# Performance work log

Hardware: AMD Instinct MI355X
Metric: run time of the kernel (lower is better)

The kernel has to match this reference:

```python
import jax, jax.numpy as jnp
from jax import lax
import numpy as np

BLOCKS = 6
DIM = 768
D_STATE = 16
D_CONV = 4
EXPAND = 2
HEADDIM = 64
D_INNER = EXPAND * DIM              # 1536
NHEADS = D_INNER // HEADDIM        # 24
CONV_DIM = D_INNER + 2 * D_STATE   # 1568 (ngroups=1)
D_IN_PROJ = 2 * D_INNER + 2 * D_STATE + NHEADS  # 3128
NPITCH = 128


def setup_inputs() -> dict:
    key = jax.random.key(0)
    ks = jax.random.split(key, 16)
    B, L = 4, 4096
    s = 0.02
    return {
        "x": jax.random.normal(ks[0], (B, L, DIM), jnp.float32),
        "type_IDs": jax.random.randint(ks[1], (B, L), 0, 2),
        "in_proj_w": jax.random.normal(ks[2], (BLOCKS, D_IN_PROJ, DIM), jnp.float32) * s,
        "conv_w": jax.random.normal(ks[3], (BLOCKS, CONV_DIM, D_CONV), jnp.float32) * 0.1,
        "conv_b": jnp.zeros((BLOCKS, CONV_DIM), jnp.float32),
        "dt_bias": jax.random.uniform(ks[4], (BLOCKS, NHEADS), jnp.float32, -4.0, -2.0),
        "A_log": jnp.tile(jnp.log(jnp.linspace(1.0, 16.0, NHEADS, dtype=jnp.float32)), (BLOCKS, 1)),
        "D": jnp.ones((BLOCKS, NHEADS), jnp.float32),
        "norm_w": jnp.ones((BLOCKS, D_INNER), jnp.float32),
        "out_proj_w": jax.random.normal(ks[5], (BLOCKS, DIM, D_INNER), jnp.float32) * s,
        "head_w": jax.random.normal(ks[6], (2, DIM, DIM), jnp.float32) * s,
        "head_b": jnp.zeros((2, DIM), jnp.float32),
        "head_out_w": jax.random.normal(ks[7], (2, 4, NPITCH, DIM), jnp.float32) * s,
        "head_out_b": jnp.zeros((2, 4, NPITCH), jnp.float32),
    }


def _mamba2_block(x, Wi, cw, cb, dtb, Alog, Dp, nw, Wo):
    B, L, _ = x.shape
    zxbcdt = jnp.einsum('bld,ed->ble', x, Wi)                 # [B,L,D_IN_PROJ]
    z = zxbcdt[..., :D_INNER]
    xBC = zxbcdt[..., D_INNER:D_INNER + CONV_DIM]
    dt = zxbcdt[..., -NHEADS:]
    # causal depthwise conv1d over time
    xc = jnp.pad(jnp.swapaxes(xBC, 1, 2), ((0, 0), (0, 0), (D_CONV - 1, 0)))
    xBC = lax.conv_general_dilated(xc, cw[:, None, :], (1,), 'VALID',
                                   feature_group_count=CONV_DIM,
                                   dimension_numbers=('NCH', 'OIH', 'NCH'))
    xBC = jax.nn.silu(jnp.swapaxes(xBC, 1, 2) + cb)            # [B,L,CONV_DIM]
    xs = xBC[..., :D_INNER].reshape(B, L, NHEADS, HEADDIM)
    Bm = xBC[..., D_INNER:D_INNER + D_STATE]                   # [B,L,N]
    Cm = xBC[..., D_INNER + D_STATE:]                          # [B,L,N]
    dt = jax.nn.softplus(dt + dtb)                             # [B,L,H]
    dA = jnp.exp(dt * (-jnp.exp(Alog)))                        # [B,L,H]
    dtx = dt[..., None] * xs                                   # [B,L,H,P]

    def step(h, inp):
        dA_t, dtx_t, B_t, C_t = inp
        h = h * dA_t[:, :, None, None] + dtx_t[..., None] * B_t[:, None, None, :]
        y = jnp.einsum('bhpn,bn->bhp', h, C_t)
        return h, y

    h0 = jnp.zeros((B, NHEADS, HEADDIM, D_STATE), x.dtype)
    mv = lambda a: jnp.moveaxis(a, 1, 0)
    _, ys = lax.scan(step, h0, (mv(dA), mv(dtx), mv(Bm), mv(Cm)))
    y = jnp.moveaxis(ys, 0, 1) + Dp[None, None, :, None] * xs   # [B,L,H,P]
    y = y.reshape(B, L, D_INNER) * jax.nn.silu(z)               # gated
    y = y * lax.rsqrt(jnp.mean(y * y, -1, keepdims=True) + 1e-5) * nw
    return jnp.einsum('bli,di->bld', y, Wo)


def _head(t, hw, hb, ow, ob):
    h = jnp.einsum('bld,ed->ble', t, hw) + hb
    velocity = jnp.einsum('bld,pd->blp', h, ow[0]) + ob[0]
    onset = jax.nn.sigmoid(jnp.einsum('bld,pd->blp', h, ow[1]) + ob[1])
    offset = jax.nn.sigmoid(jnp.einsum('bld,pd->blp', h, ow[2]) + ob[2])
    frames = jax.nn.sigmoid(jnp.einsum('bld,pd->blp', h, ow[3]) + ob[3])
    return velocity, frames, onset, offset


def reference(x, type_IDs, in_proj_w, conv_w, conv_b, dt_bias, A_log, D,
              norm_w, out_proj_w, head_w, head_b, head_out_w, head_out_b):
    for i in range(BLOCKS):
        x = _mamba2_block(x, in_proj_w[i], conv_w[i], conv_b[i], dt_bias[i],
                          A_log[i], D[i], norm_w[i], out_proj_w[i])
    cmask = (type_IDs == 0).astype(x.dtype)[..., None]
    fmask = (type_IDs == 1).astype(x.dtype)[..., None]
    cv, cf, con, coff = _head(x, head_w[0], head_b[0], head_out_w[0], head_out_b[0])
    fv, ff, fon, foff = _head(x, head_w[1], head_b[1], head_out_w[1], head_out_b[1])
    # masked (instead of ragged boolean gather) to stay jit-compatible
    return jnp.stack([cv * cmask, cf * cmask, con * cmask, coff * cmask,
                      fv * fmask, ff * fmask, fon * fmask, foff * fmask])
```

## Files before the change

kernel.cpp:

```cpp
#include <hip/hip_runtime.h>
#include <cstdint>
#include <cstddef>

#define L_SEQ   4096
#define BATCH   4
#define DIMM    768
#define D_INNER 1536
#define NHEADS  24
#define HEADDIM 64
#define D_STATE 16
#define CONVD   1568
#define D_IPROJ 3128
#define ZXP     3200
#define SEGLEN  64
#define NSEG    (L_SEQ / SEGLEN)

typedef _Float16 f16x8 __attribute__((ext_vector_type(8)));
typedef _Float16 f16x4 __attribute__((ext_vector_type(4)));
typedef float    f32x4 __attribute__((ext_vector_type(4)));

__device__ __forceinline__ void glds16(const _Float16* g, _Float16* l) {
  __builtin_amdgcn_global_load_lds(
      (__attribute__((address_space(1))) unsigned int*)g,
      (__attribute__((address_space(3))) unsigned int*)l, 16, 0, 0);
}

template <int OM>
__global__ __launch_bounds__(256, 2) void gemm_mfma(
    const _Float16* __restrict__ A, int lda,
    const _Float16* __restrict__ W,
    const float* __restrict__ bias,
    void* __restrict__ Cv, long ldc, long extra,
    int M, int N, int K,
    const int* __restrict__ tidsp, int thead)
{
  __shared__ __align__(16) char smem[33792];
  _Float16* As = (_Float16*)smem;
  _Float16* Ws = (_Float16*)(smem + 16384);
  const int tid = threadIdx.x;
  const int lane = tid & 63, wid = tid >> 6;
  const int wr = wid >> 1, wc = wid & 1;

  const int nbx = gridDim.x, nby = gridDim.y;
  const int flat = blockIdx.y * nbx + blockIdx.x;
  const int xcd = flat & 7;
  const int bidx = flat >> 3;
  const int rpx = nby >> 3;
  const int rl = bidx % rpx;
  const int ct = bidx / rpx;
  const long m0 = (long)(xcd * rpx + rl) * 128;
  const int n0 = ct * 128;

  const int la = lane & 15, lg = lane >> 4;
  const int srow = lane >> 3, schunk = lane & 7;

  f32x4 acc[4][4] = {};

  for (int k0 = 0; k0 < K; k0 += 64) {
    __syncthreads();
#pragma unroll
    for (int p = 0; p < 4; ++p) {
      const int rg = (wid << 2) + p;
      const int row = (rg << 3) + srow;
      const int scn = schunk ^ (row & 7);
      glds16(A + (m0 + row) * (long)lda + k0 + scn * 8, As + rg * 512);
      int n = n0 + row; if (n >= N) n = N - 1;
      glds16(W + (long)n * K + k0 + scn * 8, Ws + rg * 512);
    }
    asm volatile("s_waitcnt vmcnt(0)" ::: "memory");
    __syncthreads();
#pragma unroll
    for (int ks = 0; ks < 2; ++ks) {
      const int cc = ks * 4 + lg;
      f16x8 af[4], bfr[4];
#pragma unroll
      for (int i = 0; i < 4; ++i) {
        int ra = wr * 64 + i * 16 + la;
        int rb = wc * 64 + i * 16 + la;
        af[i]  = *(const f16x8*)&As[ra * 64 + ((cc ^ (ra & 7)) << 3)];
        bfr[i] = *(const f16x8*)&Ws[rb * 64 + ((cc ^ (rb & 7)) << 3)];
      }
#pragma unroll
      for (int i = 0; i < 4; ++i)
#pragma unroll
        for (int j = 0; j < 4; ++j)
          acc[i][j] = __builtin_amdgcn_mfma_f32_16x16x32_f16(af[i], bfr[j], acc[i][j], 0, 0, 0);
    }
  }

  float* epi = (float*)smem;
#pragma unroll
  for (int ph = 0; ph < 2; ++ph) {
    __syncthreads();
    if (wr == ph) {
#pragma unroll
      for (int i = 0; i < 4; ++i)
#pragma unroll
        for (int j = 0; j < 4; ++j)
#pragma unroll
          for (int r = 0; r < 4; ++r)
            epi[(i * 16 + lg * 4 + r) * 132 + wc * 64 + j * 16 + la] = acc[i][j][r];
    }
    __syncthreads();
    if (OM == 3) {
      const int q = n0 >> 7;
      const int rr = tid >> 5;
      const int ch = tid & 31;
#pragma unroll
      for (int ps = 0; ps < 8; ++ps) {
        int lrow = ps * 8 + rr;
        long gr = m0 + ph * 64 + lrow;
        float keep = (tidsp[gr] == thead) ? 1.f : 0.f;
        float4 v = *(float4*)&epi[lrow * 132 + ch * 4];
        float o[4] = {v.x, v.y, v.z, v.w};
#pragma unroll
        for (int e = 0; e < 4; ++e) {
          float vv = o[e] + bias[n0 + ch * 4 + e];
          if (q != 0) vv = 1.f / (1.f + expf(-vv));
          o[e] = vv * keep;
        }
        *(float4*)((float*)Cv + (long)q * extra + gr * 128 + ch * 4) =
            make_float4(o[0], o[1], o[2], o[3]);
      }
    } else {
      const int rr = tid >> 4;
      const int ch = tid & 15;
      const int col = n0 + ch * 8;
      float b[8] = {0.f, 0.f, 0.f, 0.f, 0.f, 0.f, 0.f, 0.f};
      if (OM == 2 && col < N) {
#pragma unroll
        for (int e = 0; e < 8; ++e) b[e] = bias[col + e];
      }
#pragma unroll
      for (int ps = 0; ps < 4; ++ps) {
        int lrow = ps * 16 + rr;
        long gr = m0 + ph * 64 + lrow;
        if (col < N) {
          float4 v0 = *(float4*)&epi[lrow * 132 + ch * 8];
          float4 v1 = *(float4*)&epi[lrow * 132 + ch * 8 + 4];
          f16x8 o = {(_Float16)(v0.x + b[0]), (_Float16)(v0.y + b[1]),
                     (_Float16)(v0.z + b[2]), (_Float16)(v0.w + b[3]),
                     (_Float16)(v1.x + b[4]), (_Float16)(v1.y + b[5]),
                     (_Float16)(v1.z + b[6]), (_Float16)(v1.w + b[7])};
          *(f16x8*)((_Float16*)Cv + gr * ldc + col) = o;
        }
      }
    }
  }
}

__global__ __launch_bounds__(256) void cvt_kernel(
    const float* __restrict__ src, _Float16* __restrict__ dst, long n4)
{
  long i = (long)blockIdx.x * 256 + threadIdx.x;
  long stride = (long)gridDim.x * 256;
  for (; i < n4; i += stride) {
    float4 v = *(const float4*)(src + i * 4);
    f16x4 o = { (_Float16)v.x, (_Float16)v.y, (_Float16)v.z, (_Float16)v.w };
    *(f16x4*)(dst + i * 4) = o;
  }
}

__global__ __launch_bounds__(256) void pack_head_kernel(
    const float* __restrict__ how, const float* __restrict__ hob,
    _Float16* __restrict__ howb, float* __restrict__ hobp)
{
  const int wmap[4] = {0, 3, 1, 2};
  int idx = blockIdx.x * 256 + threadIdx.x;
  if (idx < 2 * 512 * 768) {
    int t = idx / (512 * 768);
    int rem = idx - t * 512 * 768;
    int q = rem / (128 * 768);
    int rem2 = rem - q * 128 * 768;
    howb[idx] = (_Float16)how[((size_t)(t * 4 + wmap[q])) * 128 * 768 + rem2];
  }
  if (idx < 1024) {
    int t = idx >> 9, rem = idx & 511;
    int q = rem >> 7, pp = rem & 127;
    hobp[idx] = hob[(t * 4 + wmap[q]) * 128 + pp];
  }
}

__global__ __launch_bounds__(64) void ssdA_kernel(
    const _Float16* __restrict__ zx, const float* __restrict__ cw,
    const float* __restrict__ cb, const float* __restrict__ dtb,
    const float* __restrict__ alog, const float* __restrict__ Dv,
    _Float16* __restrict__ ybuf, _Float16* __restrict__ bcbuf,
    float* __restrict__ Hseg, float* __restrict__ cumq)
{
  __shared__ __align__(16) char sm[30720];
  _Float16* Mr = (_Float16*)sm;
  _Float16* XT = (_Float16*)(sm + 8192);
  _Float16* XC = (_Float16*)(sm + 16384);
  _Float16* BC = (_Float16*)(sm + 24832);
  float* sdt = (float*)(sm + 29952);
  float* sa  = (float*)(sm + 30208);
  float* sw  = (float*)(sm + 30464);
  const int lane = threadIdx.x;
  const int seg = blockIdx.x & (NSEG - 1);
  const int bh = blockIdx.x >> 6;
  const int h = bh % NHEADS, b = bh / NHEADS;
  const int bl0 = b * L_SEQ + seg * SEGLEN;

  _Float16* bcraw = Mr;
  for (int i = lane; i < 67 * 4; i += 64) {
    int r = i >> 2, q = (i & 3) << 3;
    f16x8 v = {};
    if (seg > 0 || r >= 3)
      v = *(const f16x8*)&zx[(size_t)(bl0 - 3 + r) * ZXP + 2 * D_INNER + q];
    *(f16x8*)&bcraw[r * 32 + q] = v;
  }
  {
    float raw = (float)zx[(size_t)(bl0 + lane) * ZXP + (D_INNER + CONVD) + h] + dtb[h];
    float sp = (raw > 20.f) ? raw : log1pf(expf(raw));
    sdt[lane] = sp;
    float av = expf(alog[h]) * sp;
#pragma unroll
    for (int off = 1; off < 64; off <<= 1) {
      float tv = __shfl_up(av, off, 64);
      if (lane >= off) av += tv;
    }
    sa[lane] = av;
    cumq[(size_t)bh * L_SEQ + seg * SEGLEN + lane] = expf(-av);
    float alast = __shfl(av, 63, 64);
    sw[lane] = expf(av - alast);
  }
  __syncthreads();

  for (int i = lane; i < SEGLEN * 32; i += 64) {
    int t = i >> 5, c = i & 31;
    float acc = cb[D_INNER + c];
#pragma unroll
    for (int k = 0; k < 4; ++k)
      acc = fmaf(cw[(D_INNER + c) * 4 + k], (float)bcraw[(t + k) * 32 + c], acc);
    float s = acc / (1.f + expf(-acc));
    _Float16 sh = (_Float16)s;
    BC[t * 40 + c] = sh;
    bcbuf[(size_t)(bl0 + t) * 32 + c] = sh;
  }
  __syncthreads();

  const int xch = h * HEADDIM + lane;
  const _Float16* xg = zx + (size_t)bl0 * ZXP + D_INNER + xch;
  const float cwx0 = cw[xch * 4 + 0], cwx1 = cw[xch * 4 + 1];
  const float cwx2 = cw[xch * 4 + 2], cwx3 = cw[xch * 4 + 3];
  const float cbx = cb[xch];
  float xw0 = 0.f, xw1 = 0.f, xw2 = 0.f;
  if (seg > 0) {
    xw0 = (float)xg[-3 * (long)ZXP];
    xw1 = (float)xg[-2 * (long)ZXP];
    xw2 = (float)xg[-1 * (long)ZXP];
  }
  float xcur = (float)xg[0];
  for (int t = 0; t < SEGLEN; ++t) {
    float xnext = (t < SEGLEN - 1) ? (float)xg[(size_t)(t + 1) * ZXP] : 0.f;
    float xa = cbx;
    xa = fmaf(cwx0, xw0, xa);
    xa = fmaf(cwx1, xw1, xa);
    xa = fmaf(cwx2, xw2, xa);
    xa = fmaf(cwx3, xcur, xa);
    float xv = xa / (1.f + expf(-xa));
    XC[t * 66 + lane] = (_Float16)xv;
    float dtx = sdt[t] * xv;
    XT[lane * 64 + ((((t >> 3) ^ (lane & 7))) << 3) + (t & 7)] = (_Float16)dtx;
    xw0 = xw1; xw1 = xw2; xw2 = xcur; xcur = xnext;
  }
  __syncthreads();

  const int la = lane & 15, lg = lane >> 4;

  f32x4 acc1[4][4] = {};
  {
    f16x8 af[4], bf[4];
#pragma unroll
    for (int i = 0; i < 4; ++i) {
      f16x8 v = {};
      if (lg < 2) v = *(const f16x8*)&BC[(i * 16 + la) * 40 + 16 + lg * 8];
      af[i] = v;
    }
#pragma unroll
    for (int j = 0; j < 4; ++j) {
      f16x8 v = {};
      if (lg < 2) v = *(const f16x8*)&BC[(j * 16 + la) * 40 + lg * 8];
      bf[j] = v;
    }
#pragma unroll
    for (int i = 0; i < 4; ++i)
#pragma unroll
      for (int j = 0; j < 4; ++j)
        acc1[i][j] = __builtin_amdgcn_mfma_f32_16x16x32_f16(af[i], bf[j], acc1[i][j], 0, 0, 0);
  }
#pragma unroll
  for (int i = 0; i < 4; ++i)
#pragma unroll
    for (int j = 0; j < 4; ++j)
#pragma unroll
      for (int r = 0; r < 4; ++r) {
        int t = i * 16 + lg * 4 + r, s = j * 16 + la;
        float m = 0.f;
        if (s <= t) m = acc1[i][j][r] * expf(sa[s] - sa[t]);
        Mr[t * 64 + ((((s >> 3) ^ (t & 7))) << 3) + (s & 7)] = (_Float16)m;
      }
  __syncthreads();

  f32x4 acc2[4][4] = {};
#pragma unroll
  for (int ks = 0; ks < 2; ++ks) {
    const int cc = ks * 4 + lg;
    f16x8 am[4], wx[4];
#pragma unroll
    for (int i = 0; i < 4; ++i) {
      int rt = i * 16 + la;
      am[i] = *(const f16x8*)&Mr[rt * 64 + ((cc ^ (rt & 7)) << 3)];
    }
#pragma unroll
    for (int j = 0; j < 4; ++j) {
      int rp = j * 16 + la;
      wx[j] = *(const f16x8*)&XT[rp * 64 + ((cc ^ (rp & 7)) << 3)];
    }
#pragma unroll
    for (int i = 0; i < 4; ++i)
#pragma unroll
      for (int j = 0; j < 4; ++j)
        acc2[i][j] = __builtin_amdgcn_mfma_f32_16x16x32_f16(am[i], wx[j], acc2[i][j], 0, 0, 0);
  }
  const float Dh = Dv[h];
#pragma unroll
  for (int i = 0; i < 4; ++i)
#pragma unroll
    for (int j = 0; j < 4; ++j)
#pragma unroll
      for (int r = 0; r < 4; ++r) {
        int t = i * 16 + lg * 4 + r, p = j * 16 + la;
        float y = acc2[i][j][r] + Dh * (float)XC[t * 66 + p];
        ybuf[(size_t)(bl0 + t) * D_INNER + h * HEADDIM + p] = (_Float16)y;
      }

  f32x4 acc3[4] = {};
#pragma unroll
  for (int ks = 0; ks < 2; ++ks) {
    const int cc = ks * 4 + lg;
    f16x8 b3;
#pragma unroll
    for (int e = 0; e < 8; ++e)
      b3[e] = BC[(ks * 32 + lg * 8 + e) * 40 + la];
#pragma unroll
    for (int i = 0; i < 4; ++i) {
      int rp = i * 16 + la;
      f16x8 a3 = *(const f16x8*)&XT[rp * 64 + ((cc ^ (rp & 7)) << 3)];
      f16x8 a3w;
#pragma unroll
      for (int e = 0; e < 8; ++e)
        a3w[e] = (_Float16)((float)a3[e] * sw[ks * 32 + lg * 8 + e]);
      acc3[i] = __builtin_amdgcn_mfma_f32_16x16x32_f16(a3w, b3, acc3[i], 0, 0, 0);
    }
  }
  float* Hst = Hseg + ((size_t)bh * NSEG + seg) * 1024;
#pragma unroll
  for (int i = 0; i < 4; ++i)
#pragma unroll
    for (int r = 0; r < 4; ++r) {
      int p = i * 16 + lg * 4 + r;
      Hst[p * 16 + la] = acc3[i][r];
    }
}

__global__ __launch_bounds__(1024) void scanB_kernel(
    float* __restrict__ Hseg, const float* __restrict__ cumq)
{
  const int bh = blockIdx.x;
  const int t = threadIdx.x;
  __shared__ float sp[NSEG];
  if (t < NSEG) sp[t] = cumq[(size_t)bh * L_SEQ + t * SEGLEN + (SEGLEN - 1)];
  __syncthreads();
  float v[NSEG];
#pragma unroll
  for (int s = 0; s < NSEG; ++s)
    v[s] = Hseg[((size_t)bh * NSEG + s) * 1024 + t];
  float h = 0.f;
#pragma unroll
  for (int s = 0; s < NSEG; ++s) {
    Hseg[((size_t)bh * NSEG + s) * 1024 + t] = h;
    h = fmaf(sp[s], h, v[s]);
  }
}

__global__ __launch_bounds__(64) void ssdC_kernel(
    _Float16* __restrict__ ybuf, const _Float16* __restrict__ bcbuf,
    const float* __restrict__ Hseg, const float* __restrict__ cumq)
{
  const int seg = blockIdx.x & (NSEG - 1);
  if (seg == 0) return;
  const int lane = threadIdx.x;
  const int bh = blockIdx.x >> 6;
  const int h = bh % NHEADS, b = bh / NHEADS;
  const int bl0 = b * L_SEQ + seg * SEGLEN;
  __shared__ float scq[SEGLEN];
  scq[lane] = cumq[(size_t)bh * L_SEQ + seg * SEGLEN + lane];
  const int la = lane & 15, lg = lane >> 4;
  const float* slot = Hseg + ((size_t)bh * NSEG + seg) * 1024;

  f16x8 a4[4], w4[4];
#pragma unroll
  for (int i = 0; i < 4; ++i) {
    f16x8 v = {};
    if (lg < 2)
      v = *(const f16x8*)&bcbuf[(size_t)(bl0 + i * 16 + la) * 32 + 16 + lg * 8];
    a4[i] = v;
  }
#pragma unroll
  for (int j = 0; j < 4; ++j) {
    f16x8 v = {};
    if (lg < 2) {
#pragma unroll
      for (int e = 0; e < 8; ++e)
        v[e] = (_Float16)slot[(j * 16 + la) * 16 + lg * 8 + e];
    }
    w4[j] = v;
  }
  f32x4 acc[4][4] = {};
#pragma unroll
  for (int i = 0; i < 4; ++i)
#pragma unroll
    for (int j = 0; j < 4; ++j)
      acc[i][j] = __builtin_amdgcn_mfma_f32_16x16x32_f16(a4[i], w4[j], acc[i][j], 0, 0, 0);
  __syncthreads();
#pragma unroll
  for (int i = 0; i < 4; ++i)
#pragma unroll
    for (int j = 0; j < 4; ++j)
#pragma unroll
      for (int r = 0; r < 4; ++r) {
        int t = i * 16 + lg * 4 + r, p = j * 16 + la;
        size_t ad = (size_t)(bl0 + t) * D_INNER + h * HEADDIM + p;
        ybuf[ad] = (_Float16)((float)ybuf[ad] + scq[t] * acc[i][j][r]);
      }
}

__global__ __launch_bounds__(256) void norm_kernel(
    const _Float16* __restrict__ y, _Float16* __restrict__ zx,
    const float* __restrict__ nw)
{
  const int row = blockIdx.x;
  const int tid = threadIdx.x;
  const _Float16* yr = y + (size_t)row * D_INNER;
  _Float16* zr = zx + (size_t)row * ZXP;
  float v[6];
  float ss = 0.f;
#pragma unroll
  for (int jj = 0; jj < 6; ++jj) {
    int c = jj * 256 + tid;
    float yv = (float)yr[c];
    float zv = (float)zr[c];
    float sz = zv / (1.f + expf(-zv));
    float val = yv * sz;
    v[jj] = val;
    ss = fmaf(val, val, ss);
  }
#pragma unroll
  for (int off = 32; off > 0; off >>= 1) ss += __shfl_xor(ss, off, 64);
  __shared__ float red[4];
  if ((tid & 63) == 0) red[tid >> 6] = ss;
  __syncthreads();
  float tot = red[0] + red[1] + red[2] + red[3];
  float rs = rsqrtf(tot * (1.f / 1536.f) + 1e-5f);
#pragma unroll
  for (int jj = 0; jj < 6; ++jj) {
    int c = jj * 256 + tid;
    zr[c] = (_Float16)(v[jj] * rs * nw[c]);
  }
}

extern "C" void kernel_launch(void* const* d_in, const int* in_sizes, int n_in,
                              void* d_out, int out_size, void* d_ws, size_t ws_size,
                              hipStream_t stream)
{
  const float* x_in = (const float*)d_in[0];
  const int*   tids = (const int*)d_in[1];
  const float* ipw  = (const float*)d_in[2];
  const float* cw   = (const float*)d_in[3];
  const float* cb   = (const float*)d_in[4];
  const float* dtb  = (const float*)d_in[5];
  const float* alog = (const float*)d_in[6];
  const float* Dv   = (const float*)d_in[7];
  const float* nw   = (const float*)d_in[8];
  const float* opw  = (const float*)d_in[9];
  const float* hw   = (const float*)d_in[10];
  const float* hb   = (const float*)d_in[11];
  const float* how  = (const float*)d_in[12];
  const float* hob  = (const float*)d_in[13];
  float* out = (float*)d_out;

  char* p = (char*)d_ws;
  _Float16* ipw_b = (_Float16*)p; p += (size_t)14413824 * 2;
  _Float16* opw_b = (_Float16*)p; p += (size_t)7077888 * 2;
  _Float16* hw_b  = (_Float16*)p; p += (size_t)1179648 * 2;
  _Float16* how_b = (_Float16*)p; p += (size_t)786432 * 2;
  float*    hob_p = (float*)p;    p += (size_t)1024 * 4;
  const size_t used_w = (size_t)(p - (char*)d_ws);
  const size_t PB = 54528000;
  int nb = 4;
  while (nb > 1 && used_w + (size_t)nb * PB > ws_size) nb >>= 1;

  cvt_kernel<<<8192, 256, 0, stream>>>(ipw, ipw_b, 14413824 / 4);
  cvt_kernel<<<6912, 256, 0, stream>>>(opw, opw_b, 7077888 / 4);
  cvt_kernel<<<1152, 256, 0, stream>>>(hw, hw_b, 1179648 / 4);
  pack_head_kernel<<<3072, 256, 0, stream>>>(how, hob, how_b, hob_p);

  for (int b0 = 0; b0 < BATCH; b0 += nb) {
    const int MT = nb * L_SEQ;
    _Float16* zx    = (_Float16*)p;
    _Float16* ybuf  = zx + (size_t)MT * ZXP;
    _Float16* bcbuf = ybuf + (size_t)MT * D_INNER;
    float*    Hseg  = (float*)(bcbuf + (size_t)MT * 32);
    float*    cumq  = Hseg + (size_t)nb * NHEADS * NSEG * 1024;
    _Float16* xbuf  = (_Float16*)(cumq + (size_t)MT * NHEADS);
    _Float16* hbuf  = zx;

    cvt_kernel<<<6144, 256, 0, stream>>>(x_in + (size_t)b0 * L_SEQ * DIMM,
                                         xbuf, (long)MT * DIMM / 4);

    for (int i = 0; i < 6; ++i) {
      gemm_mfma<0><<<dim3((D_IPROJ + 127) / 128, MT / 128), 256, 0, stream>>>(
          xbuf, DIMM, ipw_b + (size_t)i * D_IPROJ * DIMM, nullptr,
          zx, ZXP, 0, MT, D_IPROJ, DIMM, nullptr, 0);
      ssdA_kernel<<<nb * NHEADS * NSEG, 64, 0, stream>>>(
          zx, cw + (size_t)i * CONVD * 4, cb + i * CONVD,
          dtb + i * NHEADS, alog + i * NHEADS, Dv + i * NHEADS,
          ybuf, bcbuf, Hseg, cumq);
      scanB_kernel<<<nb * NHEADS, 1024, 0, stream>>>(Hseg, cumq);
      ssdC_kernel<<<nb * NHEADS * NSEG, 64, 0, stream>>>(ybuf, bcbuf, Hseg, cumq);
      norm_kernel<<<MT, 256, 0, stream>>>(ybuf, zx, nw + i * D_INNER);
      gemm_mfma<0><<<dim3(DIMM / 128, MT / 128), 256, 0, stream>>>(
          zx, ZXP, opw_b + (size_t)i * DIMM * D_INNER, nullptr,
          xbuf, DIMM, 0, MT, DIMM, D_INNER, nullptr, 0);
    }

    for (int t = 0; t < 2; ++t) {
      gemm_mfma<2><<<dim3(DIMM / 128, MT / 128), 256, 0, stream>>>(
          xbuf, DIMM, hw_b + (size_t)t * DIMM * DIMM, hb + t * DIMM,
          hbuf, DIMM, 0, MT, DIMM, DIMM, nullptr, 0);
      gemm_mfma<3><<<dim3(4, MT / 128), 256, 0, stream>>>(
          hbuf, DIMM, how_b + (size_t)t * 512 * DIMM, hob_p + t * 512,
          out + (size_t)t * 4 * 16384 * 128 + (size_t)b0 * L_SEQ * 128,
          128, (long)16384 * 128, MT, 512, DIMM,
          tids + (size_t)b0 * L_SEQ, t);
    }
  }
}
```

Baseline: 2.110 ms.

## Keep SSD intra-chunk mask in registers and shrink ssdA shared memory

The ssdA kernel now computes the masked C·B^T decay matrix with 16x16x16 MFMAs laid out so the result fragments feed the next MFMA straight from registers, removing the Mr shared-memory round trip and its barrier. The transposed dt-scaled x buffer and the separate copy of x are replaced by one XV buffer. The dt and decay scalings are applied on the fly when operands are built, with the decay weight pre-multiplied by dt. Shared memory per block drops from about 30KB to 14KB, which should allow more resident blocks. The cost is more register pressure from holding 16 fragments and more scalar conversion work when building operands.

```diff
diff --git a/kernel.cpp b/kernel.cpp
--- a/kernel.cpp
+++ b/kernel.cpp
@@ -188,21 +188,19 @@
     _Float16* __restrict__ ybuf, _Float16* __restrict__ bcbuf,
     float* __restrict__ Hseg, float* __restrict__ cumq)
 {
-  __shared__ __align__(16) char sm[30720];
-  _Float16* Mr = (_Float16*)sm;
-  _Float16* XT = (_Float16*)(sm + 8192);
-  _Float16* XC = (_Float16*)(sm + 16384);
-  _Float16* BC = (_Float16*)(sm + 24832);
-  float* sdt = (float*)(sm + 29952);
-  float* sa  = (float*)(sm + 30208);
-  float* sw  = (float*)(sm + 30464);
+  __shared__ __align__(16) char sm[14336];
+  _Float16* XV    = (_Float16*)sm;
+  _Float16* bcraw = (_Float16*)sm;
+  _Float16* BC    = (_Float16*)(sm + 8448);
+  float* sa  = (float*)(sm + 13568);
+  float* sdt = (float*)(sm + 13824);
+  float* sws = (float*)(sm + 14080);
   const int lane = threadIdx.x;
   const int seg = blockIdx.x & (NSEG - 1);
   const int bh = blockIdx.x >> 6;
   const int h = bh % NHEADS, b = bh / NHEADS;
   const int bl0 = b * L_SEQ + seg * SEGLEN;
 
-  _Float16* bcraw = Mr;
   for (int i = lane; i < 67 * 4; i += 64) {
     int r = i >> 2, q = (i & 3) << 3;
     f16x8 v = {};
@@ -223,7 +221,7 @@
     sa[lane] = av;
     cumq[(size_t)bh * L_SEQ + seg * SEGLEN + lane] = expf(-av);
     float alast = __shfl(av, 63, 64);
-    sw[lane] = expf(av - alast);
+    sws[lane] = expf(av - alast) * sp;
   }
   __syncthreads();
 
@@ -259,110 +257,93 @@
     xa = fmaf(cwx1, xw1, xa);
     xa = fmaf(cwx2, xw2, xa);
     xa = fmaf(cwx3, xcur, xa);
-    float xv = xa / (1.f + expf(-xa));
-    XC[t * 66 + lane] = (_Float16)xv;
-    float dtx = sdt[t] * xv;
-    XT[lane * 64 + ((((t >> 3) ^ (lane & 7))) << 3) + (t & 7)] = (_Float16)dtx;
+    XV[t * 66 + lane] = (_Float16)(xa / (1.f + expf(-xa)));
     xw0 = xw1; xw1 = xw2; xw2 = xcur; xcur = xnext;
   }
   __syncthreads();
 
   const int la = lane & 15, lg = lane >> 4;
 
-  f32x4 acc1[4][4] = {};
+  f16x4 Mfrag[4][4];
   {
-    f16x8 af[4], bf[4];
-#pragma unroll
-    for (int i = 0; i < 4; ++i) {
-      f16x8 v = {};
-      if (lg < 2) v = *(const f16x8*)&BC[(i * 16 + la) * 40 + 16 + lg * 8];
-      af[i] = v;
-    }
-#pragma unroll
-    for (int j = 0; j < 4; ++j) {
-      f16x8 v = {};
-      if (lg < 2) v = *(const f16x8*)&BC[(j * 16 + la) * 40 + lg * 8];
-      bf[j] = v;
-    }
-#pragma unroll
-    for (int i = 0; i < 4; ++i)
-#pragma unroll
-      for (int j = 0; j < 4; ++j)
-        acc1[i][j] = __builtin_amdgcn_mfma_f32_16x16x32_f16(af[i], bf[j], acc1[i][j], 0, 0, 0);
-  }
-#pragma unroll
-  for (int i = 0; i < 4; ++i)
-#pragma unroll
-    for (int j = 0; j < 4; ++j)
+    f16x4 cf[4];
+    float sat[4];
+#pragma unroll
+    for (int tt = 0; tt < 4; ++tt) {
+      cf[tt] = *(const f16x4*)&BC[(tt * 16 + la) * 40 + 16 + lg * 4];
+      sat[tt] = sa[tt * 16 + la];
+    }
+#pragma unroll
+    for (int st = 0; st < 4; ++st) {
+      f16x4 bfA = *(const f16x4*)&BC[(st * 16 + la) * 40 + lg * 4];
+#pragma unroll
+      for (int tt = 0; tt < 4; ++tt) {
+        f32x4 a1 = {};
+        a1 = __builtin_amdgcn_mfma_f32_16x16x16f16(bfA, cf[tt], a1, 0, 0, 0);
+        f16x4 m;
+#pragma unroll
+        for (int r = 0; r < 4; ++r) {
+          int s = st * 16 + lg * 4 + r;
+          int t = tt * 16 + la;
+          float mv = 0.f;
+          if (s <= t) mv = a1[r] * expf(sa[s] - sat[tt]);
+          m[r] = (_Float16)mv;
+        }
+        Mfrag[st][tt] = m;
+      }
+    }
+  }
+
+  f16x4 b3[4];
+#pragma unroll
+  for (int st = 0; st < 4; ++st) {
+    f16x4 v;
+#pragma unroll
+    for (int e = 0; e < 4; ++e)
+      v[e] = BC[(st * 16 + lg * 4 + e) * 40 + la];
+    b3[st] = v;
+  }
+
+  const float Dh = Dv[h];
+  float* Hst = Hseg + ((size_t)bh * NSEG + seg) * 1024;
+#pragma unroll
+  for (int pt = 0; pt < 4; ++pt) {
+    f16x4 bf[4], af3[4];
+#pragma unroll
+    for (int st = 0; st < 4; ++st) {
+      f16x4 v, w;
+#pragma unroll
+      for (int e = 0; e < 4; ++e) {
+        int s = st * 16 + lg * 4 + e;
+        float xv = (float)XV[s * 66 + pt * 16 + la];
+        v[e] = (_Float16)(xv * sdt[s]);
+        w[e] = (_Float16)(xv * sws[s]);
+      }
+      bf[st] = v; af3[st] = w;
+    }
+#pragma unroll
+    for (int tt = 0; tt < 4; ++tt) {
+      f32x4 a2 = {};
+#pragma unroll
+      for (int st = 0; st < 4; ++st)
+        a2 = __builtin_amdgcn_mfma_f32_16x16x16f16(Mfrag[st][tt], bf[st], a2, 0, 0, 0);
 #pragma unroll
       for (int r = 0; r < 4; ++r) {
-        int t = i * 16 + lg * 4 + r, s = j * 16 + la;
-        float m = 0.f;
-        if (s <= t) m = acc1[i][j][r] * expf(sa[s] - sa[t]);
-        Mr[t * 64 + ((((s >> 3) ^ (t & 7))) << 3) + (s & 7)] = (_Float16)m;
-      }
-  __syncthreads();
-
-  f32x4 acc2[4][4] = {};
-#pragma unroll
-  for (int ks = 0; ks < 2; ++ks) {
-    const int cc = ks * 4 + lg;
-    f16x8 am[4], wx[4];
-#pragma unroll
-    for (int i = 0; i < 4; ++i) {
-      int rt = i * 16 + la;
-      am[i] = *(const f16x8*)&Mr[rt * 64 + ((cc ^ (rt & 7)) << 3)];
-    }
-#pragma unroll
-    for (int j = 0; j < 4; ++j) {
-      int rp = j * 16 + la;
-      wx[j] = *(const f16x8*)&XT[rp * 64 + ((cc ^ (rp & 7)) << 3)];
-    }
-#pragma unroll
-    for (int i = 0; i < 4; ++i)
-#pragma unroll
-      for (int j = 0; j < 4; ++j)
-        acc2[i][j] = __builtin_amdgcn_mfma_f32_16x16x32_f16(am[i], wx[j], acc2[i][j], 0, 0, 0);
-  }
-  const float Dh = Dv[h];
-#pragma unroll
-  for (int i = 0; i < 4; ++i)
-#pragma unroll
-    for (int j = 0; j < 4; ++j)
-#pragma unroll
-      for (int r = 0; r < 4; ++r) {
-        int t = i * 16 + lg * 4 + r, p = j * 16 + la;
-        float y = acc2[i][j][r] + Dh * (float)XC[t * 66 + p];
+        int t = tt * 16 + lg * 4 + r, p = pt * 16 + la;
+        float y = a2[r] + Dh * (float)XV[t * 66 + p];
         ybuf[(size_t)(bl0 + t) * D_INNER + h * HEADDIM + p] = (_Float16)y;
       }
-
-  f32x4 acc3[4] = {};
-#pragma unroll
-  for (int ks = 0; ks < 2; ++ks) {
-    const int cc = ks * 4 + lg;
-    f16x8 b3;
-#pragma unroll
-    for (int e = 0; e < 8; ++e)
-      b3[e] = BC[(ks * 32 + lg * 8 + e) * 40 + la];
-#pragma unroll
-    for (int i = 0; i < 4; ++i) {
-      int rp = i * 16 + la;
-      f16x8 a3 = *(const f16x8*)&XT[rp * 64 + ((cc ^ (rp & 7)) << 3)];
-      f16x8 a3w;
-#pragma unroll
-      for (int e = 0; e < 8; ++e)
-        a3w[e] = (_Float16)((float)a3[e] * sw[ks * 32 + lg * 8 + e]);
-      acc3[i] = __builtin_amdgcn_mfma_f32_16x16x32_f16(a3w, b3, acc3[i], 0, 0, 0);
-    }
-  }
-  float* Hst = Hseg + ((size_t)bh * NSEG + seg) * 1024;
-#pragma unroll
-  for (int i = 0; i < 4; ++i)
+    }
+    f32x4 a3 = {};
+#pragma unroll
+    for (int st = 0; st < 4; ++st)
+      a3 = __builtin_amdgcn_mfma_f32_16x16x16f16(af3[st], b3[st], a3, 0, 0, 0);
 #pragma unroll
     for (int r = 0; r < 4; ++r) {
-      int p = i * 16 + lg * 4 + r;
-      Hst[p * 16 + la] = acc3[i][r];
-    }
+      int p = pt * 16 + lg * 4 + r;
+      Hst[p * 16 + la] = a3[r];
+    }
+  }
 }
 
 __global__ __launch_bounds__(1024) void scanB_kernel(
```

Measured after the change: 1.910 ms. -9.5%, faster.
